# Optimization experiments

Hardware: AMD Instinct MI355X
Metric: run time of the kernel (lower is better)

Reference implementation:

```python
import jax, jax.numpy as jnp
import numpy as np

B, H, W, DIM, WS, NH, HID = 16, 64, 64, 256, 8, 8, 1024
SHIFT = WS // 2
N = WS * WS  # tokens per window


def _rel_pos_index(ws):
    coords = np.stack(np.meshgrid(np.arange(ws), np.arange(ws), indexing='ij')).reshape(2, -1)
    rel = (coords[:, :, None] - coords[:, None, :]).transpose(1, 2, 0)  # [n,n,2]
    rel[..., 0] += ws - 1
    rel[..., 1] += ws - 1
    rel[..., 0] *= 2 * ws - 1
    return rel.sum(-1)  # [n,n] ints in [0, (2ws-1)^2)


def _attn_mask(h, w, ws, ss):
    img = np.zeros((h, w), np.float32)
    cnt = 0
    sl = (slice(0, -ws), slice(-ws, -ss), slice(-ss, None))
    for hs in sl:
        for wsl in sl:
            img[hs, wsl] = cnt
            cnt += 1
    mw = img.reshape(h // ws, ws, w // ws, ws).transpose(0, 2, 1, 3).reshape(-1, ws * ws)
    d = mw[:, None, :] - mw[:, :, None]  # unsqueeze(1) - unsqueeze(2)
    return np.where(d != 0, np.float32(-100.0), np.float32(0.0))  # [nW,n,n]


RPI = jnp.asarray(_rel_pos_index(WS).reshape(-1))          # [n*n] int
MASK = jnp.asarray(_attn_mask(H, W, WS, SHIFT))            # [nW,n,n]


def ln(x, g, b, eps):
    m = x.mean(-1, keepdims=True)
    v = x.var(-1, keepdims=True)
    return (x - m) / jnp.sqrt(v + eps) * g + b


def win_part(x, ws):
    b, h, w, c = x.shape
    x = x.reshape(b, h // ws, ws, w // ws, ws, c).transpose(0, 1, 3, 2, 4, 5)
    return x.reshape(-1, ws * ws, c)  # [b*nW, n, c]


def win_rev(win, ws, h, w):
    c = win.shape[-1]
    b = win.shape[0] // ((h // ws) * (w // ws))
    x = win.reshape(b, h // ws, w // ws, ws, ws, c).transpose(0, 1, 3, 2, 4, 5)
    return x.reshape(b, h, w, c)


def attention(xw, qkv_w, qkv_b, rpb, out_w, out_b, mask):
    Bw, n, c = xw.shape
    dh = c // NH
    scale = dh ** -0.5
    qkv = (xw @ qkv_w + qkv_b).reshape(Bw, n, 3, NH, dh).transpose(2, 0, 3, 1, 4)
    q, k, v = qkv[0], qkv[1], qkv[2]                       # [Bw,NH,n,dh]
    dots = jnp.einsum('bhid,bhjd->bhij', q, k) * scale
    bias = rpb[RPI].reshape(n, n, NH).transpose(2, 0, 1)   # [NH,n,n]
    attn = dots + bias[None]
    if mask is not None:
        nW = mask.shape[0]
        attn = attn.reshape(Bw // nW, nW, NH, n, n) + mask[None, :, None]
        attn = attn.reshape(Bw, NH, n, n)
    attn = jax.nn.softmax(attn, axis=-1)
    out = jnp.einsum('bhij,bhjd->bhid', attn, v)
    out = out.transpose(0, 2, 1, 3).reshape(Bw, n, c)
    return out @ out_w + out_b


def block(x, shifted, mask, n1g, n1b, qkv_w, qkv_b, rpb, out_w, out_b,
          n2g, n2b, lng, lnb, w1, b1, w2, b2):
    b, l, c = x.shape
    shortcut = x
    x = ln(x, n1g, n1b, 1e-5).reshape(b, H, W, c)
    if shifted:
        x = jnp.roll(x, (-SHIFT, -SHIFT), (1, 2))
    xw = win_part(x, WS)
    xw = attention(xw, qkv_w, qkv_b, rpb, out_w, out_b, mask)
    x = win_rev(xw, WS, H, W)
    if shifted:
        x = jnp.roll(x, (SHIFT, SHIFT), (1, 2))
    x = shortcut + x.reshape(b, l, c)
    # FeedForward contains its own LayerNorm(eps=1e-6) after norm2 (faithful to source)
    h = ln(x, n2g, n2b, 1e-5)
    h = ln(h, lng, lnb, 1e-6)
    h = jax.nn.gelu(h @ w1 + b1, approximate=False) @ w2 + b2
    return x + h


def forward(x, *p):
    x = block(x, False, None, *p[0:15])
    x = block(x, True, MASK, *p[15:30])
    return x


def setup_inputs() -> dict:
    key = jax.random.key(0)
    ks = iter(jax.random.split(key, 16))
    s = 0.02
    d = {'x': jax.random.normal(next(ks), (B, H * W, DIM), jnp.float32)}
    for i in (0, 1):
        p = f'b{i}_'
        d[p + 'n1g'] = jnp.ones((DIM,), jnp.float32)
        d[p + 'n1b'] = jnp.zeros((DIM,), jnp.float32)
        d[p + 'qkv_w'] = jax.random.normal(next(ks), (DIM, 3 * DIM), jnp.float32) * s
        d[p + 'qkv_b'] = jnp.zeros((3 * DIM,), jnp.float32)
        d[p + 'rpb'] = jax.random.normal(next(ks), ((2 * WS - 1) ** 2, NH), jnp.float32) * s
        d[p + 'out_w'] = jax.random.normal(next(ks), (DIM, DIM), jnp.float32) * s
        d[p + 'out_b'] = jnp.zeros((DIM,), jnp.float32)
        d[p + 'n2g'] = jnp.ones((DIM,), jnp.float32)
        d[p + 'n2b'] = jnp.zeros((DIM,), jnp.float32)
        d[p + 'lng'] = jnp.ones((DIM,), jnp.float32)
        d[p + 'lnb'] = jnp.zeros((DIM,), jnp.float32)
        d[p + 'w1'] = jax.random.normal(next(ks), (DIM, HID), jnp.float32) * s
        d[p + 'b1'] = jnp.zeros((HID,), jnp.float32)
        d[p + 'w2'] = jax.random.normal(next(ks), (HID, DIM), jnp.float32) * s
        d[p + 'b2'] = jnp.zeros((DIM,), jnp.float32)
    return d


def reference(x,
              b0_n1g, b0_n1b, b0_qkv_w, b0_qkv_b, b0_rpb, b0_out_w, b0_out_b,
              b0_n2g, b0_n2b, b0_lng, b0_lnb, b0_w1, b0_b1, b0_w2, b0_b2,
              b1_n1g, b1_n1b, b1_qkv_w, b1_qkv_b, b1_rpb, b1_out_w, b1_out_b,
              b1_n2g, b1_n2b, b1_lng, b1_lnb, b1_w1, b1_b1, b1_w2, b1_b2):
    return forward(x,
                   b0_n1g, b0_n1b, b0_qkv_w, b0_qkv_b, b0_rpb, b0_out_w, b0_out_b,
                   b0_n2g, b0_n2b, b0_lng, b0_lnb, b0_w1, b0_b1, b0_w2, b0_b2,
                   b1_n1g, b1_n1b, b1_qkv_w, b1_qkv_b, b1_rpb, b1_out_w, b1_out_b,
                   b1_n2g, b1_n2b, b1_lng, b1_lnb, b1_w1, b1_b1, b1_w2, b1_b2)
```

## Files before the change

### kernel.cpp

```cpp
#include <hip/hip_runtime.h>
#include <hip/hip_bf16.h>

typedef unsigned short u16;
typedef __attribute__((ext_vector_type(8))) short bf16x8;
typedef __attribute__((ext_vector_type(8))) unsigned short u16x8;
typedef __attribute__((ext_vector_type(4))) unsigned short u16x4;
typedef __attribute__((ext_vector_type(4))) float f32x4;

__device__ inline float b2f(u16 u) {
    union { unsigned u32; float f; } x; x.u32 = ((unsigned)u) << 16; return x.f;
}
__device__ inline u16 f2b(float f) {
    return __builtin_bit_cast(u16, __float2bfloat16(f));
}

__device__ inline float fast_gelu(float v) {
    float u = v * (2.302282f + 0.1029404f * v * v);
    return v * __builtin_amdgcn_rcpf(1.0f + __builtin_amdgcn_exp2f(-u));
}

#define GLOAD_LDS16(g, l) \
    __builtin_amdgcn_global_load_lds((const __attribute__((address_space(1))) void*)(const void*)(g), \
                                     (__attribute__((address_space(3))) void*)(void*)(l), 16, 0, 0)
#define FENCE() asm volatile("" ::: "memory")

template<int INBF16>
__global__ __launch_bounds__(256)
void ln_win_kernel(const void* __restrict__ xin, const float* __restrict__ g,
                   const float* __restrict__ b, u16* __restrict__ xw, int shift)
{
    int wid = blockIdx.x * 4 + (threadIdx.x >> 6);
    int lane = threadIdx.x & 63;
    int win = wid >> 6, tok = wid & 63;
    int bb = win >> 6, wib = win & 63;
    int h = (((wib >> 3) << 3) + (tok >> 3) + shift) & 63;
    int w = (((wib & 7) << 3) + (tok & 7) + shift) & 63;
    size_t src = ((size_t)bb * 4096 + h * 64 + w) * 256;
    float v0, v1, v2, v3;
    int c = lane * 4;
    if (INBF16) {
        u16x4 v = ((const u16x4*)((const u16*)xin + src))[lane];
        v0 = b2f(v[0]); v1 = b2f(v[1]); v2 = b2f(v[2]); v3 = b2f(v[3]);
    } else {
        float4 v = ((const float4*)((const float*)xin + src))[lane];
        v0 = v.x; v1 = v.y; v2 = v.z; v3 = v.w;
    }
    float s = v0 + v1 + v2 + v3;
    float s2 = v0*v0 + v1*v1 + v2*v2 + v3*v3;
    for (int k = 32; k > 0; k >>= 1) { s += __shfl_xor(s, k); s2 += __shfl_xor(s2, k); }
    float mean = s * (1.f/256.f);
    float var  = s2 * (1.f/256.f) - mean*mean;
    float rs = rsqrtf(var + 1e-5f);
    u16x4 o;
    o[0] = f2b((v0 - mean) * rs * g[c+0] + b[c+0]);
    o[1] = f2b((v1 - mean) * rs * g[c+1] + b[c+1]);
    o[2] = f2b((v2 - mean) * rs * g[c+2] + b[c+2]);
    o[3] = f2b((v3 - mean) * rs * g[c+3] + b[c+3]);
    *(u16x4*)(xw + (size_t)wid * 256 + c) = o;
}

__global__ __launch_bounds__(256)
void ln2_kernel(const u16* __restrict__ xin,
                const float* __restrict__ g1, const float* __restrict__ b1,
                const float* __restrict__ g2, const float* __restrict__ b2,
                u16* __restrict__ out)
{
    int wid = blockIdx.x * 4 + (threadIdx.x >> 6);
    int lane = threadIdx.x & 63;
    u16x4 v = ((const u16x4*)(xin + (size_t)wid * 256))[lane];
    float v0 = b2f(v[0]), v1 = b2f(v[1]), v2 = b2f(v[2]), v3 = b2f(v[3]);
    float s = v0 + v1 + v2 + v3;
    float s2 = v0*v0 + v1*v1 + v2*v2 + v3*v3;
    for (int k = 32; k > 0; k >>= 1) { s += __shfl_xor(s, k); s2 += __shfl_xor(s2, k); }
    float mean = s * (1.f/256.f);
    float var  = s2 * (1.f/256.f) - mean*mean;
    float rs = rsqrtf(var + 1e-5f);
    int c = lane * 4;
    float y0 = (v0 - mean) * rs * g1[c+0] + b1[c+0];
    float y1 = (v1 - mean) * rs * g1[c+1] + b1[c+1];
    float y2 = (v2 - mean) * rs * g1[c+2] + b1[c+2];
    float y3 = (v3 - mean) * rs * g1[c+3] + b1[c+3];
    float t = y0 + y1 + y2 + y3;
    float t2 = y0*y0 + y1*y1 + y2*y2 + y3*y3;
    for (int k = 32; k > 0; k >>= 1) { t += __shfl_xor(t, k); t2 += __shfl_xor(t2, k); }
    float m2 = t * (1.f/256.f);
    float vr = t2 * (1.f/256.f) - m2*m2;
    float rs2 = rsqrtf(vr + 1e-6f);
    u16x4 o;
    o[0] = f2b((y0 - m2) * rs2 * g2[c+0] + b2[c+0]);
    o[1] = f2b((y1 - m2) * rs2 * g2[c+1] + b2[c+1]);
    o[2] = f2b((y2 - m2) * rs2 * g2[c+2] + b2[c+2]);
    o[3] = f2b((y3 - m2) * rs2 * g2[c+3] + b2[c+3]);
    *(u16x4*)(out + (size_t)wid * 256 + c) = o;
}

__global__ __launch_bounds__(256)
void transpose_w(const float* __restrict__ W, u16* __restrict__ Wt, int K, int N)
{
    __shared__ float t[32][33];
    int nb = blockIdx.x * 32, kb = blockIdx.y * 32;
    int tx = threadIdx.x & 31, ty = threadIdx.x >> 5;
    #pragma unroll
    for (int r = 0; r < 32; r += 8)
        t[ty + r][tx] = W[(size_t)(kb + ty + r) * N + nb + tx];
    __syncthreads();
    #pragma unroll
    for (int r = 0; r < 32; r += 8)
        Wt[(size_t)(nb + ty + r) * K + kb + tx] = f2b(t[tx][ty + r]);
}

__global__ __launch_bounds__(256)
void build_bias(const float* __restrict__ rpb, float* __restrict__ bmT)
{
    int idx = blockIdx.x * 256 + threadIdx.x;
    int q = idx & 63, k = (idx >> 6) & 63, h = (idx >> 12) & 7, cls = idx >> 15;
    int qh = q >> 3, qw = q & 7, kh = k >> 3, kw = k & 7;
    float v = rpb[((qh - kh + 7) * 15 + (qw - kw + 7)) * 8 + h];
    int ch = cls >> 1, cw = cls & 1;
    int rq = (ch ? (qh < 4 ? 1 : 2) : 0) * 3 + (cw ? (qw < 4 ? 1 : 2) : 0);
    int rk = (ch ? (kh < 4 ? 1 : 2) : 0) * 3 + (cw ? (kw < 4 ? 1 : 2) : 0);
    if (rq != rk) v -= 100.f;
    bmT[idx] = v * 1.4426950408889634f;
}

template<int EPI, int RBF16>
__global__ __launch_bounds__(256, 2)
void areg_gemm(const u16* __restrict__ A, const u16* __restrict__ Bt,
               const float* __restrict__ bias, void* __restrict__ out,
               const void* __restrict__ resid, int N, int shift)
{
    constexpr int K = 256;
    __shared__ u16 Bs[2][8][64][32];
    const int tid = threadIdx.x, lane = tid & 63, wv = tid >> 6;
    const int g = lane >> 4, r = lane & 15;
    const int bid = blockIdx.x;
    const int bm = (bid & 7) * 64 + (bid >> 3);
    const int row0 = bm * 128 + wv * 32;

    bf16x8 af[2][8];
    #pragma unroll
    for (int rf = 0; rf < 2; ++rf)
        #pragma unroll
        for (int ks = 0; ks < 8; ++ks)
            af[rf][ks] = *(const bf16x8*)(A + (size_t)(row0 + rf * 16 + r) * K + ks * 32 + g * 8);

    const int NB = N >> 6;
#define STAGE(bn_, buf_) do { \
        _Pragma("unroll") \
        for (int it = 0; it < 8; ++it) { \
            const int S = it * 256 + wv * 64 + lane; \
            const int ks_ = S >> 8, col_ = (S >> 2) & 63; \
            const int k8_ = (S & 3) ^ (col_ & 3) ^ ((col_ >> 2) & 1); \
            GLOAD_LDS16(Bt + (size_t)((bn_) * 64 + col_) * K + ks_ * 32 + k8_ * 8, \
                        &Bs[buf_][0][0][0] + (size_t)(it * 256 + wv * 64) * 8); \
        } \
    } while (0)

    const int rc = (g ^ (r & 3) ^ ((r >> 2) & 1)) * 8;

    FENCE();
    STAGE(0, 0);
    for (int bn = 0; bn < NB; ++bn) {
        const int cur = bn & 1;
        if (bn + 1 < NB) { STAGE(bn + 1, cur ^ 1); }
        if (bn == 0) {
            asm volatile("s_waitcnt vmcnt(8)" ::: "memory");
        } else if (bn + 1 < NB) {
            if (EPI == 2) asm volatile("s_waitcnt vmcnt(24)" ::: "memory");
            else          asm volatile("s_waitcnt vmcnt(16)" ::: "memory");
        } else {
            if (EPI == 2) asm volatile("s_waitcnt vmcnt(16)" ::: "memory");
            else          asm volatile("s_waitcnt vmcnt(8)" ::: "memory");
        }
        __builtin_amdgcn_s_barrier();
        FENCE();
        f32x4 acc[4][2] = {};
        #pragma unroll
        for (int ks = 0; ks < 8; ++ks) {
            bf16x8 bf[4];
            #pragma unroll
            for (int cf = 0; cf < 4; ++cf)
                bf[cf] = *(const bf16x8*)(&Bs[cur][ks][cf * 16 + r][rc]);
            __builtin_amdgcn_s_setprio(1);
            #pragma unroll
            for (int cf = 0; cf < 4; ++cf)
                #pragma unroll
                for (int rf = 0; rf < 2; ++rf)
                    acc[cf][rf] = __builtin_amdgcn_mfma_f32_16x16x32_bf16(bf[cf], af[rf][ks], acc[cf][rf], 0, 0, 0);
            __builtin_amdgcn_s_setprio(0);
        }
        asm volatile("s_waitcnt lgkmcnt(0)" ::: "memory");
        __builtin_amdgcn_sched_barrier(0);
        #pragma unroll
        for (int rf = 0; rf < 2; ++rf) {
            const int row = row0 + rf * 16 + r;
            size_t orow;
            if (EPI == 2) {
                int win = row >> 6, tok = row & 63;
                int bb = win >> 6, wib = win & 63;
                int h = (((wib >> 3) << 3) + (tok >> 3) + shift) & 63;
                int w = (((wib & 7) << 3) + (tok & 7) + shift) & 63;
                orow = (size_t)bb * 4096 + h * 64 + w;
            } else {
                orow = (size_t)row;
            }
            #pragma unroll
            for (int cf = 0; cf < 4; ++cf) {
                const int colb = bn * 64 + cf * 16 + g * 4;
                const f32x4 bv = *(const f32x4*)(bias + colb);
                if (EPI == 0) {
                    u16x4 o;
                    #pragma unroll
                    for (int e = 0; e < 4; ++e) o[e] = f2b(acc[cf][rf][e] + bv[e]);
                    *(u16x4*)((u16*)out + (size_t)row * N + colb) = o;
                } else if (EPI == 1) {
                    u16x4 o;
                    #pragma unroll
                    for (int e = 0; e < 4; ++e) o[e] = f2b(fast_gelu(acc[cf][rf][e] + bv[e]));
                    *(u16x4*)((u16*)out + (size_t)row * N + colb) = o;
                } else {
                    float rv[4];
                    if (RBF16) {
                        const u16x4 rb = *(const u16x4*)((const u16*)resid + orow * N + colb);
                        #pragma unroll
                        for (int e = 0; e < 4; ++e) rv[e] = b2f(rb[e]);
                    } else {
                        const f32x4 rb = *(const f32x4*)((const float*)resid + orow * N + colb);
                        #pragma unroll
                        for (int e = 0; e < 4; ++e) rv[e] = rb[e];
                    }
                    u16x4 o;
                    #pragma unroll
                    for (int e = 0; e < 4; ++e) o[e] = f2b(rv[e] + acc[cf][rf][e] + bv[e]);
                    *(u16x4*)((u16*)out + orow * N + colb) = o;
                }
            }
        }
        FENCE();
        __builtin_amdgcn_s_barrier();
        FENCE();
    }
#undef STAGE
}

template<int OUTBF16>
__global__ __launch_bounds__(256)
void gemm_k4(const u16* __restrict__ A, const u16* __restrict__ Bt,
             const float* __restrict__ bias, void* __restrict__ out,
             const u16* __restrict__ resid, int M, int N, int K)
{
    __shared__ u16 As[4][128][32];
    __shared__ u16 Bs[4][128][32];
    const int tid = threadIdx.x, lane = tid & 63, wv = tid >> 6;
    const int g = lane >> 4, r = lane & 15;
    const int wr = wv >> 1, wc = wv & 1;
    const int nwg = gridDim.x * gridDim.y;
    const int lid = blockIdx.y * gridDim.x + blockIdx.x;
    const int qq = nwg >> 3, r8 = nwg & 7;
    const int xcd = lid & 7, pos = lid >> 3;
    const int nid = (xcd < r8 ? xcd * (qq + 1) : r8 * (qq + 1) + (xcd - r8) * qq) + pos;
    const int bm = nid / gridDim.x, bn = nid % gridDim.x;
    f32x4 acc[4][4] = {};
    const int arow = wv * 16 + (lane >> 2);
    const int scol = (((lane & 3) ^ ((lane >> 2) & 3) ^ ((lane >> 4) & 1)) * 8);
    const u16* gA = A + (size_t)(bm * 128 + arow) * K + scol;
    const u16* gB = Bt + (size_t)(bn * 128 + arow) * K + scol;
    const int nk = K >> 5;
    const int rc = (g ^ (r & 3) ^ ((r >> 2) & 1)) * 8;

#define STAGE(t) do { \
        u16* a_ = &As[(t) & 3][0][0]; u16* b_ = &Bs[(t) & 3][0][0]; \
        GLOAD_LDS16(gA + (size_t)(t) * 32,                    a_ + wv * 512); \
        GLOAD_LDS16(gA + (size_t)(t) * 32 + (size_t)64 * K,   a_ + 2048 + wv * 512); \
        GLOAD_LDS16(gB + (size_t)(t) * 32,                    b_ + wv * 512); \
        GLOAD_LDS16(gB + (size_t)(t) * 32 + (size_t)64 * K,   b_ + 2048 + wv * 512); \
    } while (0)

    STAGE(0);
    STAGE(1);
    for (int kt = 0; kt < nk; ++kt) {
        const int cur = kt & 3;
        if (kt + 2 < nk) {
            STAGE(kt + 2);
            asm volatile("s_waitcnt vmcnt(8)" ::: "memory");
        } else if (kt + 1 < nk) {
            asm volatile("s_waitcnt vmcnt(4)" ::: "memory");
        } else {
            asm volatile("s_waitcnt vmcnt(0)" ::: "memory");
        }
        __builtin_amdgcn_s_barrier();
        FENCE();
        bf16x8 af[4], bf[4];
        #pragma unroll
        for (int i = 0; i < 4; ++i)
            af[i] = *(const bf16x8*)(&As[cur][wr * 64 + i * 16 + r][rc]);
        #pragma unroll
        for (int j = 0; j < 4; ++j)
            bf[j] = *(const bf16x8*)(&Bs[cur][wc * 64 + j * 16 + r][rc]);
        __builtin_amdgcn_s_setprio(1);
        #pragma unroll
        for (int j = 0; j < 4; ++j)
            #pragma unroll
            for (int i = 0; i < 4; ++i)
                acc[j][i] = __builtin_amdgcn_mfma_f32_16x16x32_bf16(bf[j], af[i], acc[j][i], 0, 0, 0);
        __builtin_amdgcn_s_setprio(0);
        asm volatile("s_waitcnt lgkmcnt(0)" ::: "memory");
        __builtin_amdgcn_sched_barrier(0);
    }
#undef STAGE

    #pragma unroll
    for (int i = 0; i < 4; ++i) {
        const int row = bm * 128 + wr * 64 + i * 16 + r;
        #pragma unroll
        for (int j = 0; j < 4; ++j) {
            const int colb = bn * 128 + wc * 64 + j * 16 + g * 4;
            const f32x4 bv = *(const f32x4*)(bias + colb);
            const u16x4 rb = *(const u16x4*)(resid + (size_t)row * N + colb);
            if (OUTBF16) {
                u16x4 o;
                #pragma unroll
                for (int e = 0; e < 4; ++e) o[e] = f2b(b2f(rb[e]) + acc[j][i][e] + bv[e]);
                *(u16x4*)((u16*)out + (size_t)row * N + colb) = o;
            } else {
                f32x4 o;
                #pragma unroll
                for (int e = 0; e < 4; ++e) o[e] = b2f(rb[e]) + acc[j][i][e] + bv[e];
                *(f32x4*)((float*)out + (size_t)row * N + colb) = o;
            }
        }
    }
}

template<int SHIFTED>
__global__ __launch_bounds__(256)
void attn_mfma(const u16* __restrict__ qkv, const float* __restrict__ bmT,
               u16* __restrict__ out)
{
    __shared__ u16 pbuf[4][64 * 72];
    __shared__ u16 vbuf[4][32 * 72];
    const int tid = threadIdx.x, lane = tid & 63, wv = tid >> 6;
    const int g = lane >> 4, r = lane & 15;
    const int win = blockIdx.x;
    u16* P  = pbuf[wv];
    u16* Vt = vbuf[wv];
    const u16* base = qkv + (size_t)win * 64 * 768;
    int cls = 0;
    if (SHIFTED) {
        int wib = win & 63;
        cls = (((wib >> 3) == 7) ? 2 : 0) + (((wib & 7) == 7) ? 1 : 0);
    }
    const float sc = 0.17677669529663687f * 1.4426950408889634f;

    for (int hh = 0; hh < 2; ++hh) {
        const int h = wv * 2 + hh;
        const float* bmh = bmT + ((size_t)cls * 8 + h) * 4096;
        bf16x8 kf[4], qf[4];
        #pragma unroll
        for (int i = 0; i < 4; ++i) {
            kf[i] = *(const bf16x8*)(base + (size_t)(i * 16 + r) * 768 + 256 + h * 32 + g * 8);
            qf[i] = *(const bf16x8*)(base + (size_t)(i * 16 + r) * 768 +       h * 32 + g * 8);
        }
        #pragma unroll
        for (int d0 = 0; d0 < 32; d0 += 8) {
            u16x8 vv = *(const u16x8*)(base + (size_t)lane * 768 + 512 + h * 32 + d0);
            #pragma unroll
            for (int e = 0; e < 8; ++e) Vt[(d0 + e) * 72 + lane] = vv[e];
        }
        f32x4 acc[4][4] = {};
        #pragma unroll
        for (int i = 0; i < 4; ++i)
            #pragma unroll
            for (int j = 0; j < 4; ++j)
                acc[i][j] = __builtin_amdgcn_mfma_f32_16x16x32_bf16(kf[i], qf[j], acc[i][j], 0, 0, 0);
        #pragma unroll
        for (int i = 0; i < 4; ++i) {
            const int kb = (i * 16 + g * 4) * 64;
            #pragma unroll
            for (int j = 0; j < 4; ++j) {
                const int qq = j * 16 + r;
                #pragma unroll
                for (int rr = 0; rr < 4; ++rr)
                    acc[i][j][rr] = acc[i][j][rr] * sc + bmh[kb + rr * 64 + qq];
            }
        }
        float inv_[4];
        #pragma unroll
        for (int j = 0; j < 4; ++j) {
            float m = acc[0][j][0];
            #pragma unroll
            for (int i = 0; i < 4; ++i)
                #pragma unroll
                for (int rr = 0; rr < 4; ++rr) m = fmaxf(m, acc[i][j][rr]);
            m = fmaxf(m, __shfl_xor(m, 16));
            m = fmaxf(m, __shfl_xor(m, 32));
            float s = 0.f;
            #pragma unroll
            for (int i = 0; i < 4; ++i)
                #pragma unroll
                for (int rr = 0; rr < 4; ++rr) {
                    float p = exp2f(acc[i][j][rr] - m);
                    acc[i][j][rr] = p; s += p;
                }
            s += __shfl_xor(s, 16);
            s += __shfl_xor(s, 32);
            inv_[j] = 1.f / s;
        }
        #pragma unroll
        for (int j = 0; j < 4; ++j) {
            const float iv = inv_[j];
            #pragma unroll
            for (int i = 0; i < 4; ++i) {
                u16x4 w;
                #pragma unroll
                for (int rr = 0; rr < 4; ++rr) w[rr] = f2b(acc[i][j][rr] * iv);
                *(u16x4*)(P + (j * 16 + r) * 72 + i * 16 + g * 4) = w;
            }
        }
        f32x4 o[2][4] = {};
        #pragma unroll
        for (int ks = 0; ks < 2; ++ks) {
            bf16x8 pa[4], vb[2];
            #pragma unroll
            for (int i = 0; i < 4; ++i)
                pa[i] = *(const bf16x8*)(P + (i * 16 + r) * 72 + ks * 32 + g * 8);
            #pragma unroll
            for (int j = 0; j < 2; ++j)
                vb[j] = *(const bf16x8*)(Vt + (j * 16 + r) * 72 + ks * 32 + g * 8);
            #pragma unroll
            for (int j = 0; j < 2; ++j)
                #pragma unroll
                for (int i = 0; i < 4; ++i)
                    o[j][i] = __builtin_amdgcn_mfma_f32_16x16x32_bf16(vb[j], pa[i], o[j][i], 0, 0, 0);
        }
        u16* op = out + (size_t)win * 64 * 256 + h * 32;
        #pragma unroll
        for (int i = 0; i < 4; ++i) {
            const int qrow = i * 16 + r;
            #pragma unroll
            for (int j = 0; j < 2; ++j) {
                u16x4 w;
                #pragma unroll
                for (int rr = 0; rr < 4; ++rr) w[rr] = f2b(o[j][i][rr]);
                *(u16x4*)(op + (size_t)qrow * 256 + j * 16 + g * 4) = w;
            }
        }
    }
}

extern "C" void kernel_launch(void* const* d_in, const int* in_sizes, int n_in,
                              void* d_out, int out_size, void* d_ws, size_t ws_size,
                              hipStream_t stream)
{
    (void)in_sizes; (void)n_in; (void)out_size; (void)ws_size;
    const float* x = (const float*)d_in[0];
    char* ws = (char*)d_ws;
    size_t off = 0;
    auto alloc = [&](size_t bytes) { void* p = ws + off; off += (bytes + 255) & ~(size_t)255; return p; };

    u16 *wtq[2], *wto[2], *wt1[2], *wt2[2];
    float* bmT[2];
    for (int i = 0; i < 2; ++i) {
        wtq[i] = (u16*)alloc((size_t)768 * 256 * 2);
        wto[i] = (u16*)alloc((size_t)256 * 256 * 2);
        wt1[i] = (u16*)alloc((size_t)1024 * 256 * 2);
        wt2[i] = (u16*)alloc((size_t)256 * 1024 * 2);
        bmT[i] = (float*)alloc((size_t)4 * 8 * 64 * 64 * 4);
    }
    u16*  xw  = (u16*)alloc((size_t)65536 * 256 * 2);
    u16*  big = (u16*)alloc((size_t)65536 * 1024 * 2);
    u16*  x1b = (u16*)alloc((size_t)65536 * 256 * 2);
    u16*  xob = (u16*)alloc((size_t)65536 * 256 * 2);
    float* outp = (float*)d_out;

    for (int blk = 0; blk < 2; ++blk) {
        const float* const* P = (const float* const*)(d_in + 1 + blk * 15);
        transpose_w<<<dim3(768 / 32, 256 / 32), 256, 0, stream>>>(P[2], wtq[blk], 256, 768);
        transpose_w<<<dim3(256 / 32, 256 / 32), 256, 0, stream>>>(P[5], wto[blk], 256, 256);
        transpose_w<<<dim3(1024 / 32, 256 / 32), 256, 0, stream>>>(P[11], wt1[blk], 256, 1024);
        transpose_w<<<dim3(256 / 32, 1024 / 32), 256, 0, stream>>>(P[13], wt2[blk], 1024, 256);
        build_bias<<<512, 256, 0, stream>>>(P[4], bmT[blk]);
    }

    {
        const float* const* P = (const float* const*)(d_in + 1);
        ln_win_kernel<0><<<16384, 256, 0, stream>>>(x, P[0], P[1], xw, 0);
        areg_gemm<0, 0><<<512, 256, 0, stream>>>(xw, wtq[0], P[3], big, nullptr, 768, 0);
        attn_mfma<0><<<1024, 256, 0, stream>>>(big, bmT[0], xw);
        areg_gemm<2, 0><<<512, 256, 0, stream>>>(xw, wto[0], P[6], x1b, x, 256, 0);
        ln2_kernel<<<16384, 256, 0, stream>>>(x1b, P[7], P[8], P[9], P[10], xw);
        areg_gemm<1, 0><<<512, 256, 0, stream>>>(xw, wt1[0], P[12], big, nullptr, 1024, 0);
        gemm_k4<1><<<dim3(2, 512), 256, 0, stream>>>(big, wt2[0], P[14], xob, x1b, 65536, 256, 1024);
    }
    {
        const float* const* P = (const float* const*)(d_in + 1 + 15);
        ln_win_kernel<1><<<16384, 256, 0, stream>>>(xob, P[0], P[1], xw, 4);
        areg_gemm<0, 0><<<512, 256, 0, stream>>>(xw, wtq[1], P[3], big, nullptr, 768, 0);
        attn_mfma<1><<<1024, 256, 0, stream>>>(big, bmT[1], xw);
        areg_gemm<2, 1><<<512, 256, 0, stream>>>(xw, wto[1], P[6], x1b, xob, 256, 4);
        ln2_kernel<<<16384, 256, 0, stream>>>(x1b, P[7], P[8], P[9], P[10], xw);
        areg_gemm<1, 0><<<512, 256, 0, stream>>>(xw, wt1[1], P[12], big, nullptr, 1024, 0);
        gemm_k4<0><<<dim3(2, 512), 256, 0, stream>>>(big, wt2[1], P[14], outp, x1b, 65536, 256, 1024);
    }
}
```

Before: 624.4 us.

## Fuse double LayerNorm into MLP up-projection GEMM A-fragment prologue

Removes the standalone ln2_kernel and applies both LayerNorms (norm2, then the extra ln) inside the first MLP GEMM, working on the A-fragments already held in registers. The second norm's mean and variance are computed algebraically from per-row moment sums weighted by gamma and beta, which avoids a second read of the row. This saves one full activation read and write pass per block and a kernel launch. In exchange it adds LDS for the LN parameters, a block barrier, and extra register pressure in a kernel with launch bounds (256, 2), and the expanded variance formula may lose some precision through cancellation.

```diff
diff --git a/kernel.cpp b/kernel.cpp
--- a/kernel.cpp
+++ b/kernel.cpp
@@ -60,41 +60,6 @@
 }
 
 __global__ __launch_bounds__(256)
-void ln2_kernel(const u16* __restrict__ xin,
-                const float* __restrict__ g1, const float* __restrict__ b1,
-                const float* __restrict__ g2, const float* __restrict__ b2,
-                u16* __restrict__ out)
-{
-    int wid = blockIdx.x * 4 + (threadIdx.x >> 6);
-    int lane = threadIdx.x & 63;
-    u16x4 v = ((const u16x4*)(xin + (size_t)wid * 256))[lane];
-    float v0 = b2f(v[0]), v1 = b2f(v[1]), v2 = b2f(v[2]), v3 = b2f(v[3]);
-    float s = v0 + v1 + v2 + v3;
-    float s2 = v0*v0 + v1*v1 + v2*v2 + v3*v3;
-    for (int k = 32; k > 0; k >>= 1) { s += __shfl_xor(s, k); s2 += __shfl_xor(s2, k); }
-    float mean = s * (1.f/256.f);
-    float var  = s2 * (1.f/256.f) - mean*mean;
-    float rs = rsqrtf(var + 1e-5f);
-    int c = lane * 4;
-    float y0 = (v0 - mean) * rs * g1[c+0] + b1[c+0];
-    float y1 = (v1 - mean) * rs * g1[c+1] + b1[c+1];
-    float y2 = (v2 - mean) * rs * g1[c+2] + b1[c+2];
-    float y3 = (v3 - mean) * rs * g1[c+3] + b1[c+3];
-    float t = y0 + y1 + y2 + y3;
-    float t2 = y0*y0 + y1*y1 + y2*y2 + y3*y3;
-    for (int k = 32; k > 0; k >>= 1) { t += __shfl_xor(t, k); t2 += __shfl_xor(t2, k); }
-    float m2 = t * (1.f/256.f);
-    float vr = t2 * (1.f/256.f) - m2*m2;
-    float rs2 = rsqrtf(vr + 1e-6f);
-    u16x4 o;
-    o[0] = f2b((y0 - m2) * rs2 * g2[c+0] + b2[c+0]);
-    o[1] = f2b((y1 - m2) * rs2 * g2[c+1] + b2[c+1]);
-    o[2] = f2b((y2 - m2) * rs2 * g2[c+2] + b2[c+2]);
-    o[3] = f2b((y3 - m2) * rs2 * g2[c+3] + b2[c+3]);
-    *(u16x4*)(out + (size_t)wid * 256 + c) = o;
-}
-
-__global__ __launch_bounds__(256)
 void transpose_w(const float* __restrict__ W, u16* __restrict__ Wt, int K, int N)
 {
     __shared__ float t[32][33];
@@ -123,26 +88,30 @@
     bmT[idx] = v * 1.4426950408889634f;
 }
 
-template<int EPI, int RBF16>
+template<int EPI, int RBF16, int ALN>
 __global__ __launch_bounds__(256, 2)
 void areg_gemm(const u16* __restrict__ A, const u16* __restrict__ Bt,
                const float* __restrict__ bias, void* __restrict__ out,
-               const void* __restrict__ resid, int N, int shift)
+               const void* __restrict__ resid,
+               const float* __restrict__ lg1, const float* __restrict__ lb1,
+               const float* __restrict__ lg2, const float* __restrict__ lb2,
+               int N, int shift)
 {
     constexpr int K = 256;
     __shared__ u16 Bs[2][8][64][32];
+    __shared__ float lnp[4][256];
     const int tid = threadIdx.x, lane = tid & 63, wv = tid >> 6;
     const int g = lane >> 4, r = lane & 15;
     const int bid = blockIdx.x;
     const int bm = (bid & 7) * 64 + (bid >> 3);
     const int row0 = bm * 128 + wv * 32;
 
-    bf16x8 af[2][8];
-    #pragma unroll
-    for (int rf = 0; rf < 2; ++rf)
-        #pragma unroll
-        for (int ks = 0; ks < 8; ++ks)
-            af[rf][ks] = *(const bf16x8*)(A + (size_t)(row0 + rf * 16 + r) * K + ks * 32 + g * 8);
+    if (ALN) {
+        if (tid < 256) {
+            lnp[0][tid] = lg1[tid]; lnp[1][tid] = lb1[tid];
+            lnp[2][tid] = lg2[tid]; lnp[3][tid] = lb2[tid];
+        }
+    }
 
     const int NB = N >> 6;
 #define STAGE(bn_, buf_) do { \
@@ -156,10 +125,78 @@
         } \
     } while (0)
 
-    const int rc = (g ^ (r & 3) ^ ((r >> 2) & 1)) * 8;
-
     FENCE();
     STAGE(0, 0);
+    if (ALN) __syncthreads();
+
+    bf16x8 af[2][8];
+    #pragma unroll
+    for (int rf = 0; rf < 2; ++rf)
+        #pragma unroll
+        for (int ks = 0; ks < 8; ++ks)
+            af[rf][ks] = *(const bf16x8*)(A + (size_t)(row0 + rf * 16 + r) * K + ks * 32 + g * 8);
+
+    if (ALN) {
+        float cg = 0.f, cg2 = 0.f, cb = 0.f, cb2 = 0.f, cgb = 0.f;
+        #pragma unroll
+        for (int ks = 0; ks < 8; ++ks)
+            #pragma unroll
+            for (int e = 0; e < 8; ++e) {
+                const int c = ks * 32 + g * 8 + e;
+                const float gv = lnp[0][c], bv = lnp[1][c];
+                cg += gv; cg2 += gv * gv; cb += bv; cb2 += bv * bv; cgb += gv * bv;
+            }
+        cg  += __shfl_xor(cg, 16);  cg  += __shfl_xor(cg, 32);
+        cg2 += __shfl_xor(cg2, 16); cg2 += __shfl_xor(cg2, 32);
+        cb  += __shfl_xor(cb, 16);  cb  += __shfl_xor(cb, 32);
+        cb2 += __shfl_xor(cb2, 16); cb2 += __shfl_xor(cb2, 32);
+        cgb += __shfl_xor(cgb, 16); cgb += __shfl_xor(cgb, 32);
+        #pragma unroll
+        for (int rf = 0; rf < 2; ++rf) {
+            float s = 0.f, s2 = 0.f, sg = 0.f, sg2x = 0.f, sg2x2 = 0.f, sgbx = 0.f;
+            #pragma unroll
+            for (int ks = 0; ks < 8; ++ks) {
+                const u16x8 xp = __builtin_bit_cast(u16x8, af[rf][ks]);
+                #pragma unroll
+                for (int e = 0; e < 8; ++e) {
+                    const int c = ks * 32 + g * 8 + e;
+                    const float xv = b2f(xp[e]);
+                    const float gv = lnp[0][c], bv = lnp[1][c];
+                    s += xv; s2 += xv * xv;
+                    sg += gv * xv; sg2x += gv * gv * xv;
+                    sg2x2 += gv * gv * xv * xv; sgbx += gv * bv * xv;
+                }
+            }
+            s     += __shfl_xor(s, 16);     s     += __shfl_xor(s, 32);
+            s2    += __shfl_xor(s2, 16);    s2    += __shfl_xor(s2, 32);
+            sg    += __shfl_xor(sg, 16);    sg    += __shfl_xor(sg, 32);
+            sg2x  += __shfl_xor(sg2x, 16);  sg2x  += __shfl_xor(sg2x, 32);
+            sg2x2 += __shfl_xor(sg2x2, 16); sg2x2 += __shfl_xor(sg2x2, 32);
+            sgbx  += __shfl_xor(sgbx, 16);  sgbx  += __shfl_xor(sgbx, 32);
+            const float m1 = s * (1.f / 256.f);
+            const float rs1 = rsqrtf(s2 * (1.f / 256.f) - m1 * m1 + 1e-5f);
+            const float sumy  = rs1 * (sg - m1 * cg) + cb;
+            const float sumy2 = rs1 * rs1 * (sg2x2 - 2.f * m1 * sg2x + m1 * m1 * cg2)
+                              + 2.f * rs1 * (sgbx - m1 * cgb) + cb2;
+            const float m2 = sumy * (1.f / 256.f);
+            const float rs2 = rsqrtf(sumy2 * (1.f / 256.f) - m2 * m2 + 1e-6f);
+            #pragma unroll
+            for (int ks = 0; ks < 8; ++ks) {
+                const u16x8 xp = __builtin_bit_cast(u16x8, af[rf][ks]);
+                u16x8 op;
+                #pragma unroll
+                for (int e = 0; e < 8; ++e) {
+                    const int c = ks * 32 + g * 8 + e;
+                    const float y = (b2f(xp[e]) - m1) * rs1 * lnp[0][c] + lnp[1][c];
+                    op[e] = f2b((y - m2) * rs2 * lnp[2][c] + lnp[3][c]);
+                }
+                af[rf][ks] = __builtin_bit_cast(bf16x8, op);
+            }
+        }
+    }
+
+    const int rc = (g ^ (r & 3) ^ ((r >> 2) & 1)) * 8;
+
     for (int bn = 0; bn < NB; ++bn) {
         const int cur = bn & 1;
         if (bn + 1 < NB) { STAGE(bn + 1, cur ^ 1); }
@@ -485,21 +522,25 @@
     {
         const float* const* P = (const float* const*)(d_in + 1);
         ln_win_kernel<0><<<16384, 256, 0, stream>>>(x, P[0], P[1], xw, 0);
-        areg_gemm<0, 0><<<512, 256, 0, stream>>>(xw, wtq[0], P[3], big, nullptr, 768, 0);
+        areg_gemm<0, 0, 0><<<512, 256, 0, stream>>>(xw, wtq[0], P[3], big, nullptr,
+                                                    nullptr, nullptr, nullptr, nullptr, 768, 0);
         attn_mfma<0><<<1024, 256, 0, stream>>>(big, bmT[0], xw);
-        areg_gemm<2, 0><<<512, 256, 0, stream>>>(xw, wto[0], P[6], x1b, x, 256, 0);
-        ln2_kernel<<<16384, 256, 0, stream>>>(x1b, P[7], P[8], P[9], P[10], xw);
-        areg_gemm<1, 0><<<512, 256, 0, stream>>>(xw, wt1[0], P[12], big, nullptr, 1024, 0);
+        areg_gemm<2, 0, 0><<<512, 256, 0, stream>>>(xw, wto[0], P[6], x1b, x,
+                                                    nullptr, nullptr, nullptr, nullptr, 256, 0);
+        areg_gemm<1, 0, 1><<<512, 256, 0, stream>>>(x1b, wt1[0], P[12], big, nullptr,
+                                                    P[7], P[8], P[9], P[10], 1024, 0);
         gemm_k4<1><<<dim3(2, 512), 256, 0, stream>>>(big, wt2[0], P[14], xob, x1b, 65536, 256, 1024);
     }
     {
         const float* const* P = (const float* const*)(d_in + 1 + 15);
         ln_win_kernel<1><<<16384, 256, 0, stream>>>(xob, P[0], P[1], xw, 4);
-        areg_gemm<0, 0><<<512, 256, 0, stream>>>(xw, wtq[1], P[3], big, nullptr, 768, 0);
+        areg_gemm<0, 0, 0><<<512, 256, 0, stream>>>(xw, wtq[1], P[3], big, nullptr,
+                                                    nullptr, nullptr, nullptr, nullptr, 768, 0);
         attn_mfma<1><<<1024, 256, 0, stream>>>(big, bmT[1], xw);
-        areg_gemm<2, 1><<<512, 256, 0, stream>>>(xw, wto[1], P[6], x1b, xob, 256, 4);
-        ln2_kernel<<<16384, 256, 0, stream>>>(x1b, P[7], P[8], P[9], P[10], xw);
-        areg_gemm<1, 0><<<512, 256, 0, stream>>>(xw, wt1[1], P[12], big, nullptr, 1024, 0);
+        areg_gemm<2, 1, 0><<<512, 256, 0, stream>>>(xw, wto[1], P[6], x1b, xob,
+                                                    nullptr, nullptr, nullptr, nullptr, 256, 4);
+        areg_gemm<1, 0, 1><<<512, 256, 0, stream>>>(x1b, wt1[1], P[12], big, nullptr,
+                                                    P[7], P[8], P[9], P[10], 1024, 0);
         gemm_k4<0><<<dim3(2, 512), 256, 0, stream>>>(big, wt2[1], P[14], outp, x1b, 65536, 256, 1024);
     }
 }
```

After: 812.8 us. +30.2%, slower.
